# Optimization experiments

Hardware: AMD Instinct MI355X
Metric: run time of the kernel (lower is better)

The kernel has to match this reference:

```python
import jax, jax.numpy as jnp
import numpy as np

R = 8          # shuffle_rate
HEADS = 4
DIM_HEAD = 64


def setup_inputs() -> dict:
    key = jax.random.key(0)
    k1, k2, k3 = jax.random.split(key, 3)
    dim = 64
    C = dim * R * R            # 4096, token channel dim after unshuffle
    inner = HEADS * DIM_HEAD   # 256
    x = jax.random.normal(k1, (8, dim, 256, 256), dtype=jnp.float32)
    W_qkv = jax.random.normal(k2, (C, 3 * inner), dtype=jnp.float32) * (C ** -0.5)
    W_out = jax.random.normal(k3, (inner, C), dtype=jnp.float32) * (inner ** -0.5)
    b_out = jnp.zeros((C,), dtype=jnp.float32)
    return {"x": x, "W_qkv": W_qkv, "W_out": W_out, "b_out": b_out}


def reference(x, W_qkv, W_out, b_out):
    scale = DIM_HEAD ** -0.5
    B, C0, H0, W0 = x.shape
    h, w = H0 // R, W0 // R
    N = h * w
    C = C0 * R * R
    # PixelUnshuffle: [B,C0,H0,W0] -> [B, C0*R*R, h, w]
    xd = x.reshape(B, C0, h, R, w, R).transpose(0, 1, 3, 5, 2, 4).reshape(B, C, h, w)
    # flatten spatial -> tokens [B, N, C]
    tokens = xd.reshape(B, C, N).transpose(0, 2, 1)
    qkv = tokens @ W_qkv                                   # [B, N, 3*inner]
    q, k, v = jnp.split(qkv, 3, axis=-1)
    def heads(t):  # [B,N,inner] -> [B,H,N,d]
        return t.reshape(B, N, HEADS, DIM_HEAD).transpose(0, 2, 1, 3)
    q, k, v = heads(q), heads(k), heads(v)
    dots = jnp.einsum('bhnd,bhmd->bhnm', q, k) * scale
    attn = jax.nn.softmax(dots, axis=-1)
    out = jnp.einsum('bhnm,bhmd->bhnd', attn, v)
    out = out.transpose(0, 2, 1, 3).reshape(B, N, HEADS * DIM_HEAD)
    y = out @ W_out + b_out                                # [B, N, C]
    y = y.transpose(0, 2, 1).reshape(B, C, h, w)
    # PixelShuffle: [B, C0*R*R, h, w] -> [B, C0, H0, W0]
    y = y.reshape(B, C0, R, R, h, w).transpose(0, 1, 4, 2, 5, 3).reshape(B, C0, H0, W0)
    return y
```

## Files before the change

kernel.cpp:

```cpp
#include <hip/hip_runtime.h>

typedef unsigned short u16;
typedef __attribute__((ext_vector_type(8))) short s16x8;
typedef __attribute__((ext_vector_type(4))) short s16x4;
typedef __attribute__((ext_vector_type(4))) float f32x4;

__device__ __forceinline__ u16 f2bf(float f) {
    unsigned int u;
    __builtin_memcpy(&u, &f, 4);
    unsigned int r = u + 0x7FFFu + ((u >> 16) & 1u);
    return (u16)(r >> 16);
}

__device__ __forceinline__ unsigned int cvt_pk_bf16(float a, float b) {
    unsigned int r;
    asm("v_cvt_pk_bf16_f32 %0, %1, %2" : "=v"(r) : "v"(a), "v"(b));
    return r;
}

__device__ __forceinline__ void gl_lds16(const u16* g, u16* l) {
    __builtin_amdgcn_global_load_lds(
        (const __attribute__((address_space(1))) unsigned int*)g,
        (__attribute__((address_space(3))) unsigned int*)l,
        16, 0, 0);
}

__global__ __launch_bounds__(256) void k_transpose(const float* __restrict__ in,
                                                   u16* __restrict__ out,
                                                   int rows, int cols, int swz) {
    __shared__ float tile[64][65];
    int bx = blockIdx.x * 64, by = blockIdx.y * 64;
    int tx = threadIdx.x & 63, ty = threadIdx.x >> 6;
    for (int i = ty; i < 64; i += 4)
        tile[i][tx] = in[(size_t)(by + i) * cols + bx + tx];
    __syncthreads();
    for (int i = ty; i < 64; i += 4) {
        int n = bx + i, k = by + tx;
        int ks = swz ? (k ^ (((n >> 1) & 3) << 3)) : k;
        out[(size_t)n * rows + ks] = f2bf(tile[tx][i]);
    }
}

__global__ __launch_bounds__(512, 1) void k_gemm_qkv(const float* __restrict__ x,
                                                     const u16* __restrict__ Bt,
                                                     float* __restrict__ P) {
    __shared__ u16 As[2][256 * 32];
    __shared__ u16 Bs[2][256 * 32];
    const int tid = threadIdx.x;
    const int wave = tid >> 6, lane = tid & 63;
    const int quad = lane >> 4, l15 = lane & 15;
    const int wm = wave >> 2, wn = wave & 3;

    int lin = blockIdx.x;
    int rem = (lin & 7) * 48 + (lin >> 3);
    int tn3 = rem % 3;
    int q2  = rem / 3;
    int z   = q2 >> 5;
    int tmi = q2 & 31;
    const int tm = tmi * 256, tn = tn3 * 256;

    const int b   = tm >> 10;
    const int yy0 = (tm & 1023) >> 5;

    const int rr    = tid >> 4;
    const int col16 = tid & 15;
    const int yy_l  = rr >> 2, r1_l = rr & 3;
    const int m0    = yy_l * 32 + col16 * 2;

    u16* dstA0[2]; u16* dstA1[2];
#pragma unroll
    for (int bb = 0; bb < 2; ++bb) {
        int off0 = (m0 * 64 + r1_l * 16) ^ (((m0 >> 1) & 3) << 4);
        int off1 = ((m0 + 1) * 64 + r1_l * 16) ^ ((((m0 + 1) >> 1) & 3) << 4);
        dstA0[bb] = (u16*)((char*)As[bb] + off0);
        dstA1[bb] = (u16*)((char*)As[bb] + off1);
    }
    const float* planeBase = x + ((size_t)(b * 64)) * 65536
                               + ((yy0 + yy_l) * 8 + r1_l) * 256 + col16 * 16;

    const int brow = tid >> 2, bo = (tid & 3) * 16;
    const char* btb = (const char*)Bt;

    f32x4 acc[8][4] = {};
    float4 va[4];

    {
        const float* s = planeBase;
        s += (size_t)(z * 16) * 65536;
#pragma unroll
        for (int j = 0; j < 4; ++j) va[j] = ((const float4*)s)[j];
    }
    {
        size_t koff = (size_t)z * 2048;
        gl_lds16((const u16*)(btb + (size_t)(tn + brow) * 8192 + koff + bo),
                 Bs[0] + tid * 8);
        gl_lds16((const u16*)(btb + (size_t)(tn + 128 + brow) * 8192 + koff + bo),
                 Bs[0] + 4096 + tid * 8);
    }
    {
        uint4 pk0, pk1;
        pk0.x = cvt_pk_bf16(va[0].x, va[0].y); pk0.y = cvt_pk_bf16(va[0].z, va[0].w);
        pk0.z = cvt_pk_bf16(va[1].x, va[1].y); pk0.w = cvt_pk_bf16(va[1].z, va[1].w);
        pk1.x = cvt_pk_bf16(va[2].x, va[2].y); pk1.y = cvt_pk_bf16(va[2].z, va[2].w);
        pk1.z = cvt_pk_bf16(va[3].x, va[3].y); pk1.w = cvt_pk_bf16(va[3].z, va[3].w);
        *(uint4*)dstA0[0] = pk0;
        *(uint4*)dstA1[0] = pk1;
    }
    {
        const float* s = planeBase + (size_t)(z * 16) * 65536 + 1024;
#pragma unroll
        for (int j = 0; j < 4; ++j) va[j] = ((const float4*)s)[j];
    }
    __syncthreads();

    int cur = 0;
    for (int it = 0; it < 32; ++it) {
        if (it < 31) {
            int it1 = it + 1;
            size_t koff = (size_t)z * 2048 + (size_t)it1 * 64;
            gl_lds16((const u16*)(btb + (size_t)(tn + brow) * 8192 + koff + bo),
                     Bs[cur ^ 1] + tid * 8);
            gl_lds16((const u16*)(btb + (size_t)(tn + 128 + brow) * 8192 + koff + bo),
                     Bs[cur ^ 1] + 4096 + tid * 8);
            uint4 pk0, pk1;
            pk0.x = cvt_pk_bf16(va[0].x, va[0].y); pk0.y = cvt_pk_bf16(va[0].z, va[0].w);
            pk0.z = cvt_pk_bf16(va[1].x, va[1].y); pk0.w = cvt_pk_bf16(va[1].z, va[1].w);
            pk1.x = cvt_pk_bf16(va[2].x, va[2].y); pk1.y = cvt_pk_bf16(va[2].z, va[2].w);
            pk1.z = cvt_pk_bf16(va[3].x, va[3].y); pk1.w = cvt_pk_bf16(va[3].z, va[3].w);
            *(uint4*)dstA0[cur ^ 1] = pk0;
            *(uint4*)dstA1[cur ^ 1] = pk1;
        }
        if (it < 30) {
            int it2 = it + 2;
            const float* s = planeBase + (size_t)(z * 16 + (it2 >> 1)) * 65536
                           + (it2 & 1) * 1024;
#pragma unroll
            for (int j = 0; j < 4; ++j) va[j] = ((const float4*)s)[j];
        }
        s16x8 af[8], bf[4];
#pragma unroll
        for (int i = 0; i < 8; ++i) {
            int row = wm * 128 + i * 16 + l15;
            int off = (row * 64 + quad * 16) ^ (((row >> 1) & 3) << 4);
            af[i] = *(const s16x8*)((const char*)As[cur] + off);
        }
#pragma unroll
        for (int j = 0; j < 4; ++j) {
            int row = wn * 64 + j * 16 + l15;
            int off = (row * 64 + quad * 16) ^ (((row >> 1) & 3) << 4);
            bf[j] = *(const s16x8*)((const char*)Bs[cur] + off);
        }
        __builtin_amdgcn_s_setprio(1);
#pragma unroll
        for (int i = 0; i < 8; ++i)
#pragma unroll
            for (int j = 0; j < 4; ++j)
                acc[i][j] = __builtin_amdgcn_mfma_f32_16x16x32_bf16(af[i], bf[j], acc[i][j], 0, 0, 0);
        __builtin_amdgcn_s_setprio(0);
        __syncthreads();
        cur ^= 1;
    }

    float* Pz = P + (size_t)z * 8192 * 768;
    for (int i = 0; i < 8; ++i) {
        int mb = tm + wm * 128 + i * 16 + quad * 4;
        for (int j = 0; j < 4; ++j) {
            int col = tn + wn * 64 + j * 16 + l15;
            for (int r = 0; r < 4; ++r)
                Pz[(size_t)(mb + r) * 768 + col] = acc[i][j][r];
        }
    }
}

__global__ __launch_bounds__(256) void k_qkv_reduce(const float* __restrict__ P,
                                                    u16* __restrict__ Qo,
                                                    u16* __restrict__ Ko,
                                                    u16* __restrict__ Vt) {
    __shared__ u16 tile[64][65];
    const int tid = threadIdx.x;
    const int ct = blockIdx.x, mt = blockIdx.y;
    const int c_l = tid & 63;
    const int col = ct * 64 + c_l;
    const int mbase = mt * 64;
    const size_t NP = (size_t)8192 * 768;
    const float* P1 = P + NP;
    const float* P2 = P + 2 * NP;
    const float* P3 = P + 3 * NP;

    if (ct < 8) {
        int which = col >> 8;
        int h = (col >> 6) & 3, d = col & 63;
        u16* dst = (which == 0) ? Qo : Ko;
        for (int k = 0; k < 16; ++k) {
            int m = mbase + (tid >> 6) + k * 4;
            size_t off = (size_t)m * 768 + col;
            float v = P[off] + P1[off] + P2[off] + P3[off];
            int b = m >> 10, n = m & 1023;
            dst[((size_t)((b * 4 + h) * 1024 + n)) * 64 + d] = f2bf(v);
        }
    } else {
        int h = ct - 8;
        int b = mbase >> 10;
        int nbase = mbase & 1023;
        for (int k = 0; k < 16; ++k) {
            int ml = (tid >> 6) + k * 4;
            int m = mbase + ml;
            size_t off = (size_t)m * 768 + col;
            float v = P[off] + P1[off] + P2[off] + P3[off];
            tile[ml][c_l] = f2bf(v);
        }
        __syncthreads();
        for (int k = 0; k < 16; ++k) {
            int d = (tid >> 6) + k * 4;
            Vt[((size_t)((b * 4 + h) * 64 + d)) * 1024 + nbase + c_l] = tile[c_l][d];
        }
    }
}

__global__ __launch_bounds__(256) void k_attn(const u16* __restrict__ Qb,
                                              const u16* __restrict__ Kb,
                                              const u16* __restrict__ Vt,
                                              u16* __restrict__ aout) {
    const int bh = blockIdx.y;
    const int q0 = blockIdx.x * 64;
    const int tid = threadIdx.x;
    const int wave = tid >> 6, lane = tid & 63;
    const int quad = lane >> 4, l15 = lane & 15;
    const size_t base = (size_t)bh * 1024 * 64;
    const float scale = 0.125f;

    __shared__ u16 Ks[64 * 64];
    __shared__ u16 Vts[64 * 68];
    __shared__ u16 Ps[4][16 * 64];

    s16x8 aq0, aq1;
    {
        const u16* qp = Qb + base + (size_t)(q0 + wave * 16 + l15) * 64 + quad * 8;
        aq0 = *(const s16x8*)(qp);
        aq1 = *(const s16x8*)(qp + 32);
    }

    float m_i[4], l_i[4];
    f32x4 o[4] = {};
    for (int r = 0; r < 4; ++r) { m_i[r] = -1e30f; l_i[r] = 0.f; }

    const int vrow = tid >> 2, vpart = tid & 3;

    for (int t = 0; t < 16; ++t) {
        __syncthreads();
        for (int e = 0; e < 2; ++e) {
            int s = e * 256 + tid;
            gl_lds16(Kb + base + (size_t)t * 4096 + s * 8, Ks + s * 8);
        }
        {
            const u16* src = Vt + base + (size_t)vrow * 1024 + t * 64 + vpart * 16;
            s16x8 a = *(const s16x8*)(src);
            s16x8 b2 = *(const s16x8*)(src + 8);
            *(s16x8*)(Vts + vrow * 68 + vpart * 16) = a;
            *(s16x8*)(Vts + vrow * 68 + vpart * 16 + 8) = b2;
        }
        __syncthreads();

        f32x4 s4[4];
        for (int j = 0; j < 4; ++j) {
            const u16* kr = Ks + (j * 16 + l15) * 64 + quad * 8;
            s16x8 b0 = *(const s16x8*)(kr);
            s16x8 b1 = *(const s16x8*)(kr + 32);
            f32x4 c = {};
            c = __builtin_amdgcn_mfma_f32_16x16x32_bf16(aq0, b0, c, 0, 0, 0);
            c = __builtin_amdgcn_mfma_f32_16x16x32_bf16(aq1, b1, c, 0, 0, 0);
            s4[j] = c;
        }

        for (int r = 0; r < 4; ++r) {
            float sv0 = s4[0][r] * scale, sv1 = s4[1][r] * scale;
            float sv2 = s4[2][r] * scale, sv3 = s4[3][r] * scale;
            float mt = fmaxf(fmaxf(sv0, sv1), fmaxf(sv2, sv3));
            for (int off = 1; off < 16; off <<= 1)
                mt = fmaxf(mt, __shfl_xor(mt, off, 64));
            float mn = fmaxf(m_i[r], mt);
            float alpha = __expf(m_i[r] - mn);
            m_i[r] = mn;
            float p0 = __expf(sv0 - mn), p1 = __expf(sv1 - mn);
            float p2 = __expf(sv2 - mn), p3 = __expf(sv3 - mn);
            u16* pw = Ps[wave] + (quad * 4 + r) * 64 + l15;
            pw[0]  = f2bf(p0);
            pw[16] = f2bf(p1);
            pw[32] = f2bf(p2);
            pw[48] = f2bf(p3);
            float rs = p0 + p1 + p2 + p3;
            for (int off = 1; off < 16; off <<= 1)
                rs += __shfl_xor(rs, off, 64);
            l_i[r] = l_i[r] * alpha + rs;
            for (int dt = 0; dt < 4; ++dt) o[dt][r] *= alpha;
        }

        for (int kk = 0; kk < 64; kk += 32) {
            s16x8 pf = *(const s16x8*)(Ps[wave] + l15 * 64 + kk + quad * 8);
            for (int dt = 0; dt < 4; ++dt) {
                const u16* vr = Vts + (dt * 16 + l15) * 68 + kk + quad * 8;
                s16x4 v0 = *(const s16x4*)(vr);
                s16x4 v1 = *(const s16x4*)(vr + 4);
                s16x8 vf;
                vf[0] = v0[0]; vf[1] = v0[1]; vf[2] = v0[2]; vf[3] = v0[3];
                vf[4] = v1[0]; vf[5] = v1[1]; vf[6] = v1[2]; vf[7] = v1[3];
                o[dt] = __builtin_amdgcn_mfma_f32_16x16x32_bf16(pf, vf, o[dt], 0, 0, 0);
            }
        }
    }

    int b = bh >> 2, h = bh & 3;
    float rl[4];
    for (int r = 0; r < 4; ++r) rl[r] = 1.0f / l_i[r];
    for (int dt = 0; dt < 4; ++dt)
        for (int r = 0; r < 4; ++r) {
            int qrow = q0 + wave * 16 + quad * 4 + r;
            aout[((size_t)(b) * 1024 + qrow) * 256 + h * 64 + dt * 16 + l15] =
                f2bf(o[dt][r] * rl[r]);
        }
}

__global__ __launch_bounds__(256) void k_gemm_out(const u16* __restrict__ A,
                                                  const u16* __restrict__ Bt,
                                                  const float* __restrict__ bias,
                                                  float* __restrict__ out) {
    const int K = 256;
    __shared__ u16 As[128 * 64];
    __shared__ u16 Bs[128 * 64];
    const int tid = threadIdx.x;
    const int wave = tid >> 6, lane = tid & 63;
    const int quad = lane >> 4, l15 = lane & 15;
    const int wm = wave >> 1, wn = wave & 1;
    const int tm = blockIdx.y * 128, tn = blockIdx.x * 128;

    f32x4 acc[4][4] = {};

    for (int k0 = 0; k0 < K; k0 += 64) {
        __syncthreads();
        for (int t = 0; t < 4; ++t) {
            int c = wave * 256 + t * 64 + lane;
            int row = c >> 3, kc = c & 7;
            gl_lds16(A + (size_t)(tm + row) * K + k0 + kc * 8,
                     As + (wave * 256 + t * 64) * 8);
        }
        for (int t = 0; t < 4; ++t) {
            int c = wave * 256 + t * 64 + lane;
            int row = c >> 3, kc = c & 7;
            gl_lds16(Bt + (size_t)(tn + row) * K + k0 + kc * 8,
                     Bs + (wave * 256 + t * 64) * 8);
        }
        __syncthreads();
        for (int kk = 0; kk < 64; kk += 32) {
            s16x8 af[4], bf[4];
            for (int i = 0; i < 4; ++i)
                af[i] = *(const s16x8*)(As + (wm * 64 + i * 16 + l15) * 64 + kk + quad * 8);
            for (int j = 0; j < 4; ++j)
                bf[j] = *(const s16x8*)(Bs + (wn * 64 + j * 16 + l15) * 64 + kk + quad * 8);
            for (int i = 0; i < 4; ++i)
                for (int j = 0; j < 4; ++j)
                    acc[i][j] = __builtin_amdgcn_mfma_f32_16x16x32_bf16(af[i], bf[j], acc[i][j], 0, 0, 0);
        }
    }

    for (int i = 0; i < 4; ++i) {
        int mb = tm + wm * 64 + i * 16 + quad * 4;
        for (int j = 0; j < 4; ++j) {
            int col = tn + wn * 64 + j * 16 + l15;
            float bb = bias[col];
            int c0 = col >> 6, r1 = (col >> 3) & 7, r2 = col & 7;
            for (int r = 0; r < 4; ++r) {
                int m = mb + r;
                int b = m >> 10, n = m & 1023, yy = n >> 5, xx = n & 31;
                size_t oidx = ((size_t)((b * 64 + c0) * 256 + yy * 8 + r1)) * 256 + xx * 8 + r2;
                out[oidx] = acc[i][j][r] + bb;
            }
        }
    }
}

extern "C" void kernel_launch(void* const* d_in, const int* in_sizes, int n_in,
                              void* d_out, int out_size, void* d_ws, size_t ws_size,
                              hipStream_t stream) {
    (void)in_sizes; (void)n_in; (void)out_size; (void)ws_size;
    const float* x    = (const float*)d_in[0];
    const float* Wqkv = (const float*)d_in[1];
    const float* Wout = (const float*)d_in[2];
    const float* bout = (const float*)d_in[3];
    float* out = (float*)d_out;

    u16* ws     = (u16*)d_ws;
    u16* wqkvT  = ws;
    u16* woutT  = wqkvT + 3145728;
    u16* Qb     = woutT + 1048576;
    u16* Kb     = Qb + 2097152;
    u16* Vtb    = Kb + 2097152;
    u16* aoutb  = Vtb + 2097152;
    float* Pp   = (float*)(aoutb + 2097152);

    k_transpose<<<dim3(12, 64), 256, 0, stream>>>(Wqkv, wqkvT, 4096, 768, 1);
    k_transpose<<<dim3(64, 4), 256, 0, stream>>>(Wout, woutT, 256, 4096, 0);
    k_gemm_qkv<<<dim3(384, 1, 1), 512, 0, stream>>>(x, wqkvT, Pp);
    k_qkv_reduce<<<dim3(12, 128), 256, 0, stream>>>(Pp, Qb, Kb, Vtb);
    k_attn<<<dim3(16, 32), 256, 0, stream>>>(Qb, Kb, Vtb, aoutb);
    k_gemm_out<<<dim3(32, 64), 256, 0, stream>>>(aoutb, woutT, bout, out);
}
```

Baseline: 397.2 us.

## Triple-buffer QKV GEMM pipeline and transpose score MFMA for lane-local softmax

The QKV GEMM moves from double to triple LDS buffering. B tiles are now staged two iterations ahead, and the full __syncthreads is replaced by an lgkmcnt wait plus a raw barrier, so async global-to-LDS loads can stay in flight across iterations. Separately, the attention kernel swaps MFMA operands so each lane holds one query row's scores. This drops most of the cross-lane max/sum shuffles, and P is written as packed bf16 with an XOR swizzle. It costs more LDS in the GEMM and adds shuffles to broadcast alpha and l per output row.

```diff
diff --git a/kernel.cpp b/kernel.cpp
--- a/kernel.cpp
+++ b/kernel.cpp
@@ -44,8 +44,8 @@
 __global__ __launch_bounds__(512, 1) void k_gemm_qkv(const float* __restrict__ x,
                                                      const u16* __restrict__ Bt,
                                                      float* __restrict__ P) {
-    __shared__ u16 As[2][256 * 32];
-    __shared__ u16 Bs[2][256 * 32];
+    __shared__ u16 As[3][256 * 32];
+    __shared__ u16 Bs[3][256 * 32];
     const int tid = threadIdx.x;
     const int wave = tid >> 6, lane = tid & 63;
     const int quad = lane >> 4, l15 = lane & 15;
@@ -67,14 +67,8 @@
     const int yy_l  = rr >> 2, r1_l = rr & 3;
     const int m0    = yy_l * 32 + col16 * 2;
 
-    u16* dstA0[2]; u16* dstA1[2];
-#pragma unroll
-    for (int bb = 0; bb < 2; ++bb) {
-        int off0 = (m0 * 64 + r1_l * 16) ^ (((m0 >> 1) & 3) << 4);
-        int off1 = ((m0 + 1) * 64 + r1_l * 16) ^ ((((m0 + 1) >> 1) & 3) << 4);
-        dstA0[bb] = (u16*)((char*)As[bb] + off0);
-        dstA1[bb] = (u16*)((char*)As[bb] + off1);
-    }
+    const int aoff0 = (m0 * 64 + r1_l * 16) ^ (((m0 >> 1) & 3) << 4);
+    const int aoff1 = ((m0 + 1) * 64 + r1_l * 16) ^ ((((m0 + 1) >> 1) & 3) << 4);
     const float* planeBase = x + ((size_t)(b * 64)) * 65536
                                + ((yy0 + yy_l) * 8 + r1_l) * 256 + col16 * 16;
 
@@ -84,82 +78,87 @@
     f32x4 acc[8][4] = {};
     float4 va[4];
 
-    {
-        const float* s = planeBase;
-        s += (size_t)(z * 16) * 65536;
-#pragma unroll
-        for (int j = 0; j < 4; ++j) va[j] = ((const float4*)s)[j];
-    }
-    {
-        size_t koff = (size_t)z * 2048;
-        gl_lds16((const u16*)(btb + (size_t)(tn + brow) * 8192 + koff + bo),
-                 Bs[0] + tid * 8);
-        gl_lds16((const u16*)(btb + (size_t)(tn + 128 + brow) * 8192 + koff + bo),
-                 Bs[0] + 4096 + tid * 8);
-    }
-    {
-        uint4 pk0, pk1;
-        pk0.x = cvt_pk_bf16(va[0].x, va[0].y); pk0.y = cvt_pk_bf16(va[0].z, va[0].w);
-        pk0.z = cvt_pk_bf16(va[1].x, va[1].y); pk0.w = cvt_pk_bf16(va[1].z, va[1].w);
-        pk1.x = cvt_pk_bf16(va[2].x, va[2].y); pk1.y = cvt_pk_bf16(va[2].z, va[2].w);
-        pk1.z = cvt_pk_bf16(va[3].x, va[3].y); pk1.w = cvt_pk_bf16(va[3].z, va[3].w);
-        *(uint4*)dstA0[0] = pk0;
-        *(uint4*)dstA1[0] = pk1;
-    }
-    {
-        const float* s = planeBase + (size_t)(z * 16) * 65536 + 1024;
-#pragma unroll
-        for (int j = 0; j < 4; ++j) va[j] = ((const float4*)s)[j];
-    }
-    __syncthreads();
-
-    int cur = 0;
-    for (int it = 0; it < 32; ++it) {
-        if (it < 31) {
-            int it1 = it + 1;
-            size_t koff = (size_t)z * 2048 + (size_t)it1 * 64;
-            gl_lds16((const u16*)(btb + (size_t)(tn + brow) * 8192 + koff + bo),
-                     Bs[cur ^ 1] + tid * 8);
-            gl_lds16((const u16*)(btb + (size_t)(tn + 128 + brow) * 8192 + koff + bo),
-                     Bs[cur ^ 1] + 4096 + tid * 8);
-            uint4 pk0, pk1;
-            pk0.x = cvt_pk_bf16(va[0].x, va[0].y); pk0.y = cvt_pk_bf16(va[0].z, va[0].w);
-            pk0.z = cvt_pk_bf16(va[1].x, va[1].y); pk0.w = cvt_pk_bf16(va[1].z, va[1].w);
-            pk1.x = cvt_pk_bf16(va[2].x, va[2].y); pk1.y = cvt_pk_bf16(va[2].z, va[2].w);
-            pk1.z = cvt_pk_bf16(va[3].x, va[3].y); pk1.w = cvt_pk_bf16(va[3].z, va[3].w);
-            *(uint4*)dstA0[cur ^ 1] = pk0;
-            *(uint4*)dstA1[cur ^ 1] = pk1;
-        }
-        if (it < 30) {
-            int it2 = it + 2;
-            const float* s = planeBase + (size_t)(z * 16 + (it2 >> 1)) * 65536
-                           + (it2 & 1) * 1024;
-#pragma unroll
-            for (int j = 0; j < 4; ++j) va[j] = ((const float4*)s)[j];
-        }
-        s16x8 af[8], bf[4];
-#pragma unroll
-        for (int i = 0; i < 8; ++i) {
-            int row = wm * 128 + i * 16 + l15;
-            int off = (row * 64 + quad * 16) ^ (((row >> 1) & 3) << 4);
-            af[i] = *(const s16x8*)((const char*)As[cur] + off);
-        }
-#pragma unroll
-        for (int j = 0; j < 4; ++j) {
-            int row = wn * 64 + j * 16 + l15;
-            int off = (row * 64 + quad * 16) ^ (((row >> 1) & 3) << 4);
-            bf[j] = *(const s16x8*)((const char*)Bs[cur] + off);
-        }
-        __builtin_amdgcn_s_setprio(1);
-#pragma unroll
-        for (int i = 0; i < 8; ++i)
-#pragma unroll
-            for (int j = 0; j < 4; ++j)
-                acc[i][j] = __builtin_amdgcn_mfma_f32_16x16x32_bf16(af[i], bf[j], acc[i][j], 0, 0, 0);
-        __builtin_amdgcn_s_setprio(0);
-        __syncthreads();
-        cur ^= 1;
-    }
+#define STAGE_B(IT, BUF)                                                       \
+    {                                                                          \
+        size_t koff = (size_t)z * 2048 + (size_t)(IT) * 64;                    \
+        gl_lds16((const u16*)(btb + (size_t)(tn + brow) * 8192 + koff + bo),   \
+                 Bs[BUF] + tid * 8);                                           \
+        gl_lds16((const u16*)(btb + (size_t)(tn + 128 + brow) * 8192 + koff + bo), \
+                 Bs[BUF] + 4096 + tid * 8);                                    \
+    }
+#define LOAD_VA(IT)                                                            \
+    {                                                                          \
+        const float* s_ = planeBase + (size_t)(z * 16 + ((IT) >> 1)) * 65536   \
+                        + ((IT) & 1) * 1024;                                   \
+        va[0] = ((const float4*)s_)[0]; va[1] = ((const float4*)s_)[1];        \
+        va[2] = ((const float4*)s_)[2]; va[3] = ((const float4*)s_)[3];        \
+    }
+#define WRITE_A(BUF)                                                           \
+    {                                                                          \
+        uint4 pk0, pk1;                                                        \
+        pk0.x = cvt_pk_bf16(va[0].x, va[0].y); pk0.y = cvt_pk_bf16(va[0].z, va[0].w); \
+        pk0.z = cvt_pk_bf16(va[1].x, va[1].y); pk0.w = cvt_pk_bf16(va[1].z, va[1].w); \
+        pk1.x = cvt_pk_bf16(va[2].x, va[2].y); pk1.y = cvt_pk_bf16(va[2].z, va[2].w); \
+        pk1.z = cvt_pk_bf16(va[3].x, va[3].y); pk1.w = cvt_pk_bf16(va[3].z, va[3].w); \
+        *(uint4*)((char*)As[BUF] + aoff0) = pk0;                               \
+        *(uint4*)((char*)As[BUF] + aoff1) = pk1;                               \
+    }
+#define COMPUTE(BUF)                                                           \
+    {                                                                          \
+        s16x8 af[8], bf[4];                                                    \
+        _Pragma("unroll")                                                      \
+        for (int i = 0; i < 8; ++i) {                                          \
+            int row = wm * 128 + i * 16 + l15;                                 \
+            int off = (row * 64 + quad * 16) ^ (((row >> 1) & 3) << 4);        \
+            af[i] = *(const s16x8*)((const char*)As[BUF] + off);               \
+        }                                                                      \
+        _Pragma("unroll")                                                      \
+        for (int j = 0; j < 4; ++j) {                                          \
+            int row = wn * 64 + j * 16 + l15;                                  \
+            int off = (row * 64 + quad * 16) ^ (((row >> 1) & 3) << 4);        \
+            bf[j] = *(const s16x8*)((const char*)Bs[BUF] + off);               \
+        }                                                                      \
+        __builtin_amdgcn_s_setprio(1);                                         \
+        _Pragma("unroll")                                                      \
+        for (int i = 0; i < 8; ++i)                                            \
+            _Pragma("unroll")                                                  \
+            for (int j = 0; j < 4; ++j)                                        \
+                acc[i][j] = __builtin_amdgcn_mfma_f32_16x16x32_bf16(af[i], bf[j], acc[i][j], 0, 0, 0); \
+        __builtin_amdgcn_s_setprio(0);                                         \
+    }
+#define SOFT_BAR()                                                             \
+    {                                                                          \
+        asm volatile("s_waitcnt lgkmcnt(0)" ::: "memory");                     \
+        __builtin_amdgcn_s_barrier();                                          \
+    }
+
+    STAGE_B(0, 0);
+    LOAD_VA(0);
+    WRITE_A(0);
+    STAGE_B(1, 1);
+    LOAD_VA(1);
+    SOFT_BAR();
+
+    int c0i = 0, c1i = 1, c2i = 2;
+    for (int it = 0; it < 30; ++it) {
+        STAGE_B(it + 2, c2i);
+        WRITE_A(c1i);
+        LOAD_VA(it + 2);
+        COMPUTE(c0i);
+        SOFT_BAR();
+        int t_ = c0i; c0i = c1i; c1i = c2i; c2i = t_;
+    }
+    WRITE_A(c1i);
+    COMPUTE(c0i);
+    SOFT_BAR();
+    { int t_ = c0i; c0i = c1i; c1i = c2i; c2i = t_; }
+    COMPUTE(c0i);
+
+#undef STAGE_B
+#undef LOAD_VA
+#undef WRITE_A
+#undef COMPUTE
+#undef SOFT_BAR
 
     float* Pz = P + (size_t)z * 8192 * 768;
     for (int i = 0; i < 8; ++i) {
@@ -240,11 +239,13 @@
         aq1 = *(const s16x8*)(qp + 32);
     }
 
-    float m_i[4], l_i[4];
+    float m_i = -1e30f, l_i = 0.f;
     f32x4 o[4] = {};
-    for (int r = 0; r < 4; ++r) { m_i[r] = -1e30f; l_i[r] = 0.f; }
 
     const int vrow = tid >> 2, vpart = tid & 3;
+    char* PsW = (char*)Ps[wave];
+    const int psb  = l15 * 128;
+    const int pswz = (l15 & 7) << 4;
 
     for (int t = 0; t < 16; ++t) {
         __syncthreads();
@@ -267,36 +268,47 @@
             s16x8 b0 = *(const s16x8*)(kr);
             s16x8 b1 = *(const s16x8*)(kr + 32);
             f32x4 c = {};
-            c = __builtin_amdgcn_mfma_f32_16x16x32_bf16(aq0, b0, c, 0, 0, 0);
-            c = __builtin_amdgcn_mfma_f32_16x16x32_bf16(aq1, b1, c, 0, 0, 0);
+            c = __builtin_amdgcn_mfma_f32_16x16x32_bf16(b0, aq0, c, 0, 0, 0);
+            c = __builtin_amdgcn_mfma_f32_16x16x32_bf16(b1, aq1, c, 0, 0, 0);
             s4[j] = c;
         }
 
+        float x0 = fmaxf(fmaxf(s4[0][0], s4[0][1]), fmaxf(s4[0][2], s4[0][3]));
+        float x1 = fmaxf(fmaxf(s4[1][0], s4[1][1]), fmaxf(s4[1][2], s4[1][3]));
+        float x2 = fmaxf(fmaxf(s4[2][0], s4[2][1]), fmaxf(s4[2][2], s4[2][3]));
+        float x3 = fmaxf(fmaxf(s4[3][0], s4[3][1]), fmaxf(s4[3][2], s4[3][3]));
+        float mt = fmaxf(fmaxf(x0, x1), fmaxf(x2, x3)) * scale;
+        mt = fmaxf(mt, __shfl_xor(mt, 16, 64));
+        mt = fmaxf(mt, __shfl_xor(mt, 32, 64));
+        float mn = fmaxf(m_i, mt);
+        float alpha = __expf(m_i - mn);
+        m_i = mn;
+
+        float rs = 0.f;
+#pragma unroll
+        for (int j = 0; j < 4; ++j) {
+            float p0 = __expf(s4[j][0] * scale - mn);
+            float p1 = __expf(s4[j][1] * scale - mn);
+            float p2 = __expf(s4[j][2] * scale - mn);
+            float p3 = __expf(s4[j][3] * scale - mn);
+            rs += (p0 + p1) + (p2 + p3);
+            uint2 pk;
+            pk.x = cvt_pk_bf16(p0, p1);
+            pk.y = cvt_pk_bf16(p2, p3);
+            *(uint2*)(PsW + psb + ((j * 32 + quad * 8) ^ pswz)) = pk;
+        }
+        rs += __shfl_xor(rs, 16, 64);
+        rs += __shfl_xor(rs, 32, 64);
+        l_i = l_i * alpha + rs;
+
+#pragma unroll
         for (int r = 0; r < 4; ++r) {
-            float sv0 = s4[0][r] * scale, sv1 = s4[1][r] * scale;
-            float sv2 = s4[2][r] * scale, sv3 = s4[3][r] * scale;
-            float mt = fmaxf(fmaxf(sv0, sv1), fmaxf(sv2, sv3));
-            for (int off = 1; off < 16; off <<= 1)
-                mt = fmaxf(mt, __shfl_xor(mt, off, 64));
-            float mn = fmaxf(m_i[r], mt);
-            float alpha = __expf(m_i[r] - mn);
-            m_i[r] = mn;
-            float p0 = __expf(sv0 - mn), p1 = __expf(sv1 - mn);
-            float p2 = __expf(sv2 - mn), p3 = __expf(sv3 - mn);
-            u16* pw = Ps[wave] + (quad * 4 + r) * 64 + l15;
-            pw[0]  = f2bf(p0);
-            pw[16] = f2bf(p1);
-            pw[32] = f2bf(p2);
-            pw[48] = f2bf(p3);
-            float rs = p0 + p1 + p2 + p3;
-            for (int off = 1; off < 16; off <<= 1)
-                rs += __shfl_xor(rs, off, 64);
-            l_i[r] = l_i[r] * alpha + rs;
-            for (int dt = 0; dt < 4; ++dt) o[dt][r] *= alpha;
+            float ar = __shfl(alpha, (lane & 48) | (quad * 4 + r), 64);
+            o[0][r] *= ar; o[1][r] *= ar; o[2][r] *= ar; o[3][r] *= ar;
         }
 
         for (int kk = 0; kk < 64; kk += 32) {
-            s16x8 pf = *(const s16x8*)(Ps[wave] + l15 * 64 + kk + quad * 8);
+            s16x8 pf = *(const s16x8*)(PsW + psb + ((kk * 2 + quad * 16) ^ pswz));
             for (int dt = 0; dt < 4; ++dt) {
                 const u16* vr = Vts + (dt * 16 + l15) * 68 + kk + quad * 8;
                 s16x4 v0 = *(const s16x4*)(vr);
@@ -311,7 +323,9 @@
 
     int b = bh >> 2, h = bh & 3;
     float rl[4];
-    for (int r = 0; r < 4; ++r) rl[r] = 1.0f / l_i[r];
+#pragma unroll
+    for (int r = 0; r < 4; ++r)
+        rl[r] = 1.0f / __shfl(l_i, (lane & 48) | (quad * 4 + r), 64);
     for (int dt = 0; dt < 4; ++dt)
         for (int r = 0; r < 4; ++r) {
             int qrow = q0 + wave * 16 + quad * 4 + r;
```

Result: slower. 422.0 us (+6.2%).
